# Kernel tuning notes

Measured on AMD Instinct MI355X. Metric: run time of the kernel, lower is better.

The kernel has to match this reference:

```python
import jax, jax.numpy as jnp
import numpy as np

B, T, D = 1, 2048, 2560
H, KV, HD = 8, 4, 256
G = H // KV
S = 8192          # max_seq_len / cache length
PREV = 4096       # tokens already in cache before this chunk
SCALE = 256.0 ** -0.5   # query_pre_attn_scalar ** -0.5
EPS = 1e-6
ROPE_BASE = 10000.0


def _rmsnorm(x, scale):
    xf = x.astype(jnp.float32)
    var = jnp.mean(xf * xf, axis=-1, keepdims=True)
    return xf * jax.lax.rsqrt(var + EPS) * (1.0 + scale)


def _rope(x, cos, sin):
    # x: (b, h, t, hd); cos/sin: (t, hd)
    h = x.shape[-1] // 2
    x1, x2 = x[..., :h], x[..., h:]
    rot = jnp.concatenate([-x2, x1], axis=-1)
    return x * cos[None, None] + rot * sin[None, None]


def setup_inputs() -> dict:
    key = jax.random.key(0)
    ks = jax.random.split(key, 9)
    x = jax.random.normal(ks[0], (B, T, D), jnp.float32)
    Wq = jax.random.normal(ks[1], (H * HD, D), jnp.float32) * 0.02
    Wk = jax.random.normal(ks[2], (KV * HD, D), jnp.float32) * 0.02
    Wv = jax.random.normal(ks[3], (KV * HD, D), jnp.float32) * 0.02
    Wo = jax.random.normal(ks[4], (D, H * HD), jnp.float32) * 0.02
    q_scale = jnp.zeros((HD,), jnp.float32)
    k_scale = jnp.zeros((HD,), jnp.float32)
    k_cache = jax.random.normal(ks[5], (B, S, KV, HD), jnp.float32) * 0.02
    v_cache = jax.random.normal(ks[6], (B, S, KV, HD), jnp.float32) * 0.02
    pos = jnp.arange(PREV, PREV + T, dtype=jnp.int32)
    inv_freq = 1.0 / (ROPE_BASE ** (jnp.arange(0, HD, 2, dtype=jnp.float32) / HD))
    ang = pos.astype(jnp.float32)[:, None] * inv_freq[None, :]   # (T, HD//2)
    cos = jnp.concatenate([jnp.cos(ang), jnp.cos(ang)], axis=-1)  # (T, HD)
    sin = jnp.concatenate([jnp.sin(ang), jnp.sin(ang)], axis=-1)
    # causal mask over the full cache: True = masked out
    mask = jnp.arange(S, dtype=jnp.int32)[None, :] > pos[:, None]  # (T, S) bool
    return dict(x=x, Wq=Wq, Wk=Wk, Wv=Wv, Wo=Wo, q_scale=q_scale,
                k_scale=k_scale, k_cache=k_cache, v_cache=v_cache,
                cos=cos, sin=sin, input_positions=pos, mask=mask)


def reference(x, Wq, Wk, Wv, Wo, q_scale, k_scale, k_cache, v_cache,
              cos, sin, input_positions, mask):
    b, t, _ = x.shape
    q = (x @ Wq.T).reshape(b, t, H, HD).transpose(0, 2, 1, 3)   # (b,H,t,hd)
    k = (x @ Wk.T).reshape(b, t, KV, HD).transpose(0, 2, 1, 3)  # (b,KV,t,hd)
    v = (x @ Wv.T).reshape(b, t, KV, HD).transpose(0, 2, 1, 3)
    q = _rmsnorm(q, q_scale)
    k = _rmsnorm(k, k_scale)
    q = _rope(q, cos, sin)
    k = _rope(k, cos, sin)
    # scatter new K/V into cache at input_positions
    kc = k_cache.at[:, input_positions].set(k.transpose(0, 2, 1, 3))  # (b,S,KV,hd)
    vc = v_cache.at[:, input_positions].set(v.transpose(0, 2, 1, 3))
    # GQA attention without materializing repeated K/V: group heads by KV group
    qg = (q * SCALE).reshape(b, KV, G, t, HD)
    scores = jnp.einsum('bgntd,bsgd->bgnts', qg, kc)  # (b,KV,G,t,S)
    scores = jnp.where(mask, -jnp.inf, scores)        # broadcast (t,S)
    weights = jax.nn.softmax(scores, axis=-1)
    ctx = jnp.einsum('bgnts,bsgd->bgntd', weights, vc)  # (b,KV,G,t,hd)
    ctx = ctx.reshape(b, H, t, HD).transpose(0, 2, 1, 3).reshape(b, t, H * HD)
    return ctx @ Wo.T
```

## Files before the change

### kernel.cpp

```cpp
#include <hip/hip_runtime.h>
#include <hip/hip_bf16.h>

#define T_ 2048
#define D_ 2560
#define H_ 8
#define KV_ 4
#define HD_ 256
#define S_ 8192
#define PREV_ 4096
#define SEFF_ 6144
#define NT_ 192
#define NS_ 2
#define TPS_ 96
#define CHT_ 8
#define SCALE_ 0.0625f
#define LOG2E_ 1.44269504088896f

typedef __attribute__((ext_vector_type(8))) short short8;
typedef __attribute__((ext_vector_type(4))) float floatx4;

__device__ inline short8 ld8(const __hip_bfloat16* p) { return *(const short8*)p; }
__device__ inline short8 ld8(const float* p) {
    float4 a = *(const float4*)p;
    float4 b = *(const float4*)(p + 4);
    union { short8 s; __hip_bfloat16 h[8]; } u;
    u.h[0] = __hip_bfloat16(a.x); u.h[1] = __hip_bfloat16(a.y);
    u.h[2] = __hip_bfloat16(a.z); u.h[3] = __hip_bfloat16(a.w);
    u.h[4] = __hip_bfloat16(b.x); u.h[5] = __hip_bfloat16(b.y);
    u.h[6] = __hip_bfloat16(b.z); u.h[7] = __hip_bfloat16(b.w);
    return u.s;
}

__device__ inline short bfbits(float x) {
    __hip_bfloat16 h(x);
    short s;
    __builtin_memcpy(&s, &h, 2);
    return s;
}

__device__ inline float b2f(short u) {
    unsigned int x = ((unsigned int)(unsigned short)u) << 16;
    float f; __builtin_memcpy(&f, &x, 4); return f;
}

__device__ __forceinline__ void gld_lds(const short* g, short* l) {
    __builtin_amdgcn_global_load_lds(
        (const __attribute__((address_space(1))) unsigned int*)(const void*)g,
        (__attribute__((address_space(3))) unsigned int*)(void*)l,
        16, 0, 0);
}

__device__ __forceinline__ int kslot(int row, int c) {
    int kk = c >> 2, qd = c & 3, hf = row >> 4, lrr = row & 15;
    return (kk * 2 + hf) * 64 + ((qd * 16 + lrr) ^ kk);
}
__device__ __forceinline__ int vslot(int d, int c) {
    int ni = d >> 4, lrr = d & 15;
    return ni * 64 + ((c * 16 + lrr) ^ (ni & 7));
}

__global__ __launch_bounds__(256) void gemm_qkv(const float* __restrict__ A,
                                                const float* __restrict__ Wq,
                                                const float* __restrict__ Wk,
                                                const float* __restrict__ Wv,
                                                float* __restrict__ qo,
                                                float* __restrict__ ko,
                                                float* __restrict__ vo) {
    __shared__ __align__(16) __hip_bfloat16 As[128 * 40];
    __shared__ __align__(16) __hip_bfloat16 Bs[128 * 40];
    const int K = D_;
    const int tid = threadIdx.x;
    const int bm = (int)blockIdx.y * 128, bn = (int)blockIdx.x * 128;
    const int w = tid >> 6, lane = tid & 63, quad = lane >> 4, lr = lane & 15;
    const int wm = (w >> 1) * 64, wn = (w & 1) * 64;
    floatx4 acc[4][4] = {};
    const int row = tid >> 2;
    const int col = (tid & 3) * 8;

    const float* Bp; float* Co; int nb, ldo;
    if (bn < 2048)      { Bp = Wq + (size_t)bn * K;          Co = qo; nb = bn;        ldo = 2048; }
    else if (bn < 3072) { Bp = Wk + (size_t)(bn - 2048) * K; Co = ko; nb = bn - 2048; ldo = 1024; }
    else                { Bp = Wv + (size_t)(bn - 3072) * K; Co = vo; nb = bn - 3072; ldo = 1024; }

    for (int k0 = 0; k0 < K; k0 += 32) {
        __syncthreads();
        for (int p = 0; p < 2; ++p) {
            int r = row + p * 64;
            *(short8*)(&As[r * 40 + col]) = ld8(&A[(size_t)(bm + r) * K + k0 + col]);
            *(short8*)(&Bs[r * 40 + col]) = ld8(&Bp[(size_t)r * K + k0 + col]);
        }
        __syncthreads();
        short8 a[4], b[4];
        for (int mi = 0; mi < 4; ++mi)
            a[mi] = *(const short8*)(&As[(wm + mi * 16 + lr) * 40 + quad * 8]);
        for (int ni = 0; ni < 4; ++ni)
            b[ni] = *(const short8*)(&Bs[(wn + ni * 16 + lr) * 40 + quad * 8]);
        for (int mi = 0; mi < 4; ++mi)
            for (int ni = 0; ni < 4; ++ni)
                acc[mi][ni] = __builtin_amdgcn_mfma_f32_16x16x32_bf16(a[mi], b[ni], acc[mi][ni], 0, 0, 0);
    }
    for (int mi = 0; mi < 4; ++mi)
        for (int ni = 0; ni < 4; ++ni)
            for (int r = 0; r < 4; ++r) {
                int m = bm + wm + mi * 16 + quad * 4 + r;
                int n = nb + wn + ni * 16 + lr;
                Co[(size_t)m * ldo + n] = acc[mi][ni][r];
            }
}

__global__ __launch_bounds__(256) void gemm_wo(const __hip_bfloat16* __restrict__ A,
                                               const float* __restrict__ Bm,
                                               float* __restrict__ C) {
    __shared__ __align__(16) __hip_bfloat16 As[64 * 40];
    __shared__ __align__(16) __hip_bfloat16 Bs[128 * 40];
    const int K = 2048, N = D_;
    const int tid = threadIdx.x;
    const int bm = (int)blockIdx.y * 64, bn = (int)blockIdx.x * 128;
    const int w = tid >> 6, lane = tid & 63, quad = lane >> 4, lr = lane & 15;
    const int wn = w * 32;
    floatx4 acc[4][2] = {};
    const int row = tid >> 2;
    const int col = (tid & 3) * 8;

    for (int k0 = 0; k0 < K; k0 += 32) {
        __syncthreads();
        *(short8*)(&As[row * 40 + col]) = ld8(&A[(size_t)(bm + row) * K + k0 + col]);
        for (int p = 0; p < 2; ++p) {
            int r = row + p * 64;
            *(short8*)(&Bs[r * 40 + col]) = ld8(&Bm[(size_t)(bn + r) * K + k0 + col]);
        }
        __syncthreads();
        short8 a[4], b[2];
        for (int mi = 0; mi < 4; ++mi)
            a[mi] = *(const short8*)(&As[(mi * 16 + lr) * 40 + quad * 8]);
        for (int ni = 0; ni < 2; ++ni)
            b[ni] = *(const short8*)(&Bs[(wn + ni * 16 + lr) * 40 + quad * 8]);
        for (int mi = 0; mi < 4; ++mi)
            for (int ni = 0; ni < 2; ++ni)
                acc[mi][ni] = __builtin_amdgcn_mfma_f32_16x16x32_bf16(a[mi], b[ni], acc[mi][ni], 0, 0, 0);
    }
    for (int mi = 0; mi < 4; ++mi)
        for (int ni = 0; ni < 2; ++ni)
            for (int r = 0; r < 4; ++r) {
                int m = bm + mi * 16 + quad * 4 + r;
                int n = bn + wn + ni * 16 + lr;
                C[(size_t)m * N + n] = acc[mi][ni][r];
            }
}

__global__ __launch_bounds__(256) void norm_rope_q(const float* __restrict__ src,
                                                   const float* __restrict__ scale,
                                                   const float* __restrict__ cosd,
                                                   const float* __restrict__ sind,
                                                   __hip_bfloat16* __restrict__ dst) {
    const int rowid = blockIdx.x;
    const int t = rowid / H_, hh = rowid % H_;
    const int d = threadIdx.x;
    __shared__ float ybuf[256];
    __shared__ float wsum[4];
    float x = src[(size_t)t * (H_ * 256) + hh * 256 + d];
    float ss = x * x;
    for (int m = 1; m < 64; m <<= 1) ss += __shfl_xor(ss, m);
    if ((d & 63) == 0) wsum[d >> 6] = ss;
    __syncthreads();
    float tot = wsum[0] + wsum[1] + wsum[2] + wsum[3];
    float inv = rsqrtf(tot * (1.0f / 256.0f) + 1e-6f);
    float y = x * inv * (1.0f + scale[d]);
    ybuf[d] = y;
    __syncthreads();
    float rot = (d < 128) ? -ybuf[d + 128] : ybuf[d - 128];
    float cv = cosd[(size_t)t * 256 + d];
    float sv = sind[(size_t)t * 256 + d];
    float out = y * cv + rot * sv;
    dst[((size_t)hh * T_ + t) * 256 + d] = __hip_bfloat16(out);
}

__global__ __launch_bounds__(256) void norm_rope_k(const float* __restrict__ src,
                                                   const float* __restrict__ scale,
                                                   const float* __restrict__ cosd,
                                                   const float* __restrict__ sind,
                                                   short* __restrict__ Kp) {
    const int rowid = blockIdx.x;
    const int t = rowid / KV_, g = rowid % KV_;
    const int d = threadIdx.x;
    __shared__ float ybuf[256];
    __shared__ float wsum[4];
    float x = src[(size_t)t * (KV_ * 256) + g * 256 + d];
    float ss = x * x;
    for (int m = 1; m < 64; m <<= 1) ss += __shfl_xor(ss, m);
    if ((d & 63) == 0) wsum[d >> 6] = ss;
    __syncthreads();
    float tot = wsum[0] + wsum[1] + wsum[2] + wsum[3];
    float inv = rsqrtf(tot * (1.0f / 256.0f) + 1e-6f);
    float y = x * inv * (1.0f + scale[d]);
    ybuf[d] = y;
    __syncthreads();
    float rot = (d < 128) ? -ybuf[d + 128] : ybuf[d - 128];
    float cv = cosd[(size_t)t * 256 + d];
    float sv = sind[(size_t)t * 256 + d];
    float out = y * cv + rot * sv;
    const int s = t + PREV_;
    const int tile = s >> 5, row = s & 31;
    Kp[((size_t)(g * NT_ + tile) * 1024 + kslot(row, d >> 3)) * 8 + (d & 7)] = bfbits(out);
}

__global__ __launch_bounds__(256) void merge_k(const float* __restrict__ kin,
                                               short* __restrict__ Kp) {
    const int tile = blockIdx.x;
    const int g = blockIdx.y;
    const int s0 = tile * 32;
    const int tid = threadIdx.x;
    short* dst = Kp + (size_t)(g * NT_ + tile) * 1024 * 8;
    for (int p = 0; p < 4; ++p) {
        int cid = p * 256 + tid;
        int row = cid >> 5, c = cid & 31;
        short8 v = ld8(&kin[((size_t)(s0 + row) * KV_ + g) * 256 + c * 8]);
        *(short8*)&dst[(size_t)kslot(row, c) * 8] = v;
    }
}

__global__ __launch_bounds__(256) void transpose_v(const float* __restrict__ vin,
                                                   const float* __restrict__ vnew,
                                                   short* __restrict__ Vp) {
    __shared__ short tile[64][65];
    const int g = blockIdx.z;
    const int d0 = blockIdx.y * 64;
    const int s0 = blockIdx.x * 64;
    const int tid = threadIdx.x;
    for (int p = 0; p < 16; ++p) {
        int idx = p * 256 + tid;
        int r = idx >> 6, cc = idx & 63;
        int s = s0 + r, d = d0 + cc;
        float v;
        if (s < PREV_) v = vin[((size_t)s * KV_ + g) * 256 + d];
        else           v = vnew[(size_t)(s - PREV_) * 1024 + g * 256 + d];
        tile[r][cc] = bfbits(v);
    }
    __syncthreads();
    for (int p = 0; p < 16; ++p) {
        int idx = p * 256 + tid;
        int r = idx >> 6, cc = idx & 63;
        int s = s0 + cc, d = d0 + r;
        int tl = s >> 5, jj = s & 31;
        Vp[((size_t)(g * NT_ + tl) * 1024 + vslot(d, jj >> 3)) * 8 + (jj & 7)] = tile[cc][r];
    }
}

__global__ void init_bar(unsigned* bar) {
    if (threadIdx.x < 8 * 32) bar[threadIdx.x] = 0u;
}

__device__ __forceinline__ void gbar(unsigned* bar, int myq, unsigned target) {
    __syncthreads();
    if (threadIdx.x == 0) {
        __threadfence();
        atomicAdd(&bar[myq * 32], 1u);
        unsigned sum = 0;
        for (int i = 0; i < 8; ++i)
            sum += __hip_atomic_load(&bar[i * 32], __ATOMIC_RELAXED, __HIP_MEMORY_SCOPE_AGENT);
        while (sum < target) {
            __builtin_amdgcn_s_sleep(8);
            sum = 0;
            for (int i = 0; i < 8; ++i)
                sum += __hip_atomic_load(&bar[i * 32], __ATOMIC_RELAXED, __HIP_MEMORY_SCOPE_AGENT);
        }
    }
    __syncthreads();
}

__global__ __launch_bounds__(256, 2) void attn(const __hip_bfloat16* __restrict__ Qr,
                                               const short* __restrict__ Kp,
                                               const short* __restrict__ Vp,
                                               short* __restrict__ Po,
                                               float* __restrict__ Pm,
                                               float* __restrict__ Pl,
                                               unsigned* __restrict__ bar) {
    __shared__ __align__(16) short Ks[2][8192];
    __shared__ __align__(16) short Vs[2][8192];
    __shared__ __align__(16) short Pls[4][512];
    const int b = (int)blockIdx.x;
    const int h = b >> 6;
    const int jq = (b >> 1) & 31;
    const int ns = b & 1;
    const int g = h >> 1;
    const int qbase = jq * 64;
    const int tid = threadIdx.x;
    const int w = tid >> 6, lane = tid & 63, quad = lane >> 4, lr = lane & 15;
    const int t0 = qbase + w * 16;
    const int myq = b & 7;
    const int rot = b & (CHT_ - 1);

    const short* Qb = (const short*)Qr + ((size_t)h * T_ + t0) * 256;
    const short* Kg = Kp + (size_t)g * NT_ * 8192;
    const short* Vg = Vp + (size_t)g * NT_ * 8192;

    short8 aq[8];
    for (int kk = 0; kk < 8; ++kk)
        aq[kk] = *(const short8*)(&Qb[(size_t)lr * 256 + kk * 32 + quad * 8]);

    floatx4 o[16] = {};
    floatx4 lacc = {0.f, 0.f, 0.f, 0.f};
    float mrow[4] = {-3e38f, -3e38f, -3e38f, -3e38f};
    const float c = SCALE_ * LOG2E_;
    short* pw = &Pls[w][0];
    const short oneb = (short)0x3F80;
    const short8 ones8 = {oneb, oneb, oneb, oneb, oneb, oneb, oneb, oneb};

    const int nf_w = (PREV_ + t0) >> 5;
    const int nf_b = (PREV_ + qbase + 48) >> 5;
    const int cbeg = (ns * TPS_) / CHT_;
    const int cend = cbeg + TPS_ / CHT_;

#define STAGE_TILE(buf, tileidx) do {                                          \
        const short* Kt_ = Kg + (size_t)(tileidx) * 8192;                      \
        const short* Vt_ = Vg + (size_t)(tileidx) * 8192;                      \
        for (int p_ = 0; p_ < 4; ++p_) {                                       \
            gld_lds(Kt_ + (p_ * 256 + w * 64 + lane) * 8,                      \
                    &Ks[buf][(p_ * 256 + w * 64) * 8]);                        \
            gld_lds(Vt_ + (p_ * 256 + w * 64 + lane) * 8,                      \
                    &Vs[buf][(p_ * 256 + w * 64) * 8]);                        \
        }                                                                      \
    } while (0)

    {
        const int tf = cbeg * CHT_ + rot;
        if (tf <= nf_b) STAGE_TILE(0, tf);
    }
    int cur = 0;
    unsigned nbar = 0;
    for (int ci = cbeg; ci < cend; ++ci) {
        for (int i = 0; i < CHT_; ++i) {
            const int tile = ci * CHT_ + ((i + rot) & (CHT_ - 1));
            if (i == 0 && ci > cbeg) { ++nbar; gbar(bar, myq, 512u * nbar); }
            else __syncthreads();
            {
                int ni_ = i + 1, nc_ = ci;
                if (ni_ == CHT_) { ni_ = 0; ++nc_; }
                if (nc_ < cend) {
                    const int nt_ = nc_ * CHT_ + ((ni_ + rot) & (CHT_ - 1));
                    if (nt_ <= nf_b) STAGE_TILE(cur ^ 1, nt_);
                }
            }

            if (tile <= nf_w) {
                const int s0 = tile * 32;
                const bool masked = (tile == nf_w);
                const short* Kb = &Ks[cur][0];
                const short* Vb = &Vs[cur][0];

                floatx4 sc[2];
                __builtin_amdgcn_s_setprio(1);
                for (int half = 0; half < 2; ++half) {
                    floatx4 accs = {0.f, 0.f, 0.f, 0.f};
                    for (int kk = 0; kk < 8; ++kk) {
                        short8 bk = *(const short8*)&Kb[((kk * 2 + half) * 64 + ((quad * 16 + lr) ^ kk)) * 8];
                        accs = __builtin_amdgcn_mfma_f32_16x16x32_bf16(aq[kk], bk, accs, 0, 0, 0);
                    }
                    sc[half] = accs;
                }
                __builtin_amdgcn_s_setprio(0);
                float mnew[4];
                for (int r = 0; r < 4; ++r) {
                    float v0 = sc[0][r] * c, v1 = sc[1][r] * c;
                    if (masked) {
                        int limit = PREV_ + t0 + quad * 4 + r;
                        if (s0 + lr > limit)       v0 = -3e38f;
                        if (s0 + 16 + lr > limit)  v1 = -3e38f;
                    }
                    sc[0][r] = v0; sc[1][r] = v1;
                    float mx = fmaxf(v0, v1);
                    mx = fmaxf(mx, __shfl_xor(mx, 1));
                    mx = fmaxf(mx, __shfl_xor(mx, 2));
                    mx = fmaxf(mx, __shfl_xor(mx, 4));
                    mx = fmaxf(mx, __shfl_xor(mx, 8));
                    mnew[r] = fmaxf(mrow[r], mx);
                }
                float alpha[4];
                for (int r = 0; r < 4; ++r) { alpha[r] = exp2f(mrow[r] - mnew[r]); mrow[r] = mnew[r]; }
                for (int r = 0; r < 4; ++r) {
                    sc[0][r] = exp2f(sc[0][r] - mnew[r]);
                    sc[1][r] = exp2f(sc[1][r] - mnew[r]);
                }
                bool need = (alpha[0] < 1.f) | (alpha[1] < 1.f) | (alpha[2] < 1.f) | (alpha[3] < 1.f);
                if (__any(need)) {
                    for (int ni = 0; ni < 16; ++ni)
                        for (int r = 0; r < 4; ++r) o[ni][r] *= alpha[r];
                    for (int r = 0; r < 4; ++r) lacc[r] *= alpha[r];
                }
                for (int half = 0; half < 2; ++half)
                    for (int r = 0; r < 4; ++r) {
                        int koff2 = half * 16 + lr;
                        pw[((koff2 >> 3) * 16 + quad * 4 + r) * 8 + (koff2 & 7)] = bfbits(sc[half][r]);
                    }
                __asm__ volatile("s_waitcnt lgkmcnt(0)" ::: "memory");
                short8 ap = *(const short8*)&pw[(quad * 16 + lr) * 8];
                __builtin_amdgcn_s_setprio(1);
                lacc = __builtin_amdgcn_mfma_f32_16x16x32_bf16(ap, ones8, lacc, 0, 0, 0);
                for (int ni = 0; ni < 16; ++ni) {
                    short8 bv = *(const short8*)&Vb[(ni * 64 + ((quad * 16 + lr) ^ (ni & 7))) * 8];
                    o[ni] = __builtin_amdgcn_mfma_f32_16x16x32_bf16(ap, bv, o[ni], 0, 0, 0);
                }
                __builtin_amdgcn_s_setprio(0);
            }
            cur ^= 1;
        }
    }
#undef STAGE_TILE

    const int tq = jq * 4 + w;
    const size_t pb16 = (((size_t)h * 128 + tq) * NS_ + ns) * 16;
    const size_t pb = pb16 * 256;
    for (int ni = 0; ni < 16; ++ni) {
        union { unsigned long long u; short s4[4]; } pk;
        for (int r = 0; r < 4; ++r) pk.s4[r] = bfbits(o[ni][r]);
        *(unsigned long long*)&Po[pb + (size_t)ni * 256 + lane * 4] = pk.u;
    }
    if (lr == 0)
        for (int r = 0; r < 4; ++r) {
            Pm[pb16 + quad * 4 + r] = mrow[r];
            Pl[pb16 + quad * 4 + r] = lacc[r];
        }
}

__global__ __launch_bounds__(256) void attn_combine(const short* __restrict__ Po,
                                                    const float* __restrict__ Pm,
                                                    const float* __restrict__ Pl,
                                                    __hip_bfloat16* __restrict__ ctx) {
    const int h = blockIdx.x;
    const int tt = blockIdx.y;
    const int tid = threadIdx.x;
    __shared__ float wgt[NS_][16];
    const size_t b = ((size_t)h * 128 + tt) * NS_;
    if (tid < 16) {
        const int row = tid;
        float m[NS_], l[NS_];
        float M = -3e38f;
        for (int ns = 0; ns < NS_; ++ns) {
            m[ns] = Pm[(b + ns) * 16 + row];
            l[ns] = Pl[(b + ns) * 16 + row];
            M = fmaxf(M, m[ns]);
        }
        float denom = 0.f, wv[NS_];
        for (int ns = 0; ns < NS_; ++ns) {
            wv[ns] = exp2f(m[ns] - M);
            denom += wv[ns] * l[ns];
        }
        float rd = 1.f / denom;
        for (int ns = 0; ns < NS_; ++ns) wgt[ns][row] = wv[ns] * rd;
    }
    __syncthreads();
    const int d = tid;
    const int ni = d >> 4, dl = d & 15;
    for (int row = 0; row < 16; ++row) {
        float acc = 0.f;
        const size_t ib = (size_t)ni * 256 + ((row >> 2) * 16 + dl) * 4 + (row & 3);
        for (int ns = 0; ns < NS_; ++ns)
            acc += wgt[ns][row] * b2f(Po[(b + ns) * 4096 + ib]);
        int t = tt * 16 + row;
        ctx[(size_t)t * (H_ * 256) + h * 256 + d] = __hip_bfloat16(acc);
    }
}

extern "C" void kernel_launch(void* const* d_in, const int* in_sizes, int n_in,
                              void* d_out, int out_size, void* d_ws, size_t ws_size,
                              hipStream_t stream) {
    const float* x       = (const float*)d_in[0];
    const float* Wq      = (const float*)d_in[1];
    const float* Wk      = (const float*)d_in[2];
    const float* Wv      = (const float*)d_in[3];
    const float* Wo      = (const float*)d_in[4];
    const float* q_scale = (const float*)d_in[5];
    const float* k_scale = (const float*)d_in[6];
    const float* k_cache = (const float*)d_in[7];
    const float* v_cache = (const float*)d_in[8];
    const float* cosd    = (const float*)d_in[9];
    const float* sind    = (const float*)d_in[10];
    float* out = (float*)d_out;

    char* p = (char*)d_ws;
    float* q_f32 = (float*)p;            p += (size_t)T_ * 2048 * 4;
    float* k_f32 = (float*)p;            p += (size_t)T_ * 1024 * 4;
    float* v_f32 = (float*)p;            p += (size_t)T_ * 1024 * 4;
    __hip_bfloat16* Qr = (__hip_bfloat16*)p;  p += (size_t)H_ * T_ * 256 * 2;
    short* Kp = (short*)p;               p += (size_t)KV_ * NT_ * 1024 * 8 * 2;
    short* Vp = (short*)p;               p += (size_t)KV_ * NT_ * 1024 * 8 * 2;
    __hip_bfloat16* ctx = (__hip_bfloat16*)p; p += (size_t)T_ * 2048 * 2;
    float* Pm = (float*)p;               p += (size_t)H_ * 128 * NS_ * 16 * 4;
    float* Pl = (float*)p;               p += (size_t)H_ * 128 * NS_ * 16 * 4;
    unsigned* bar = (unsigned*)p;        p += 8 * 32 * sizeof(unsigned);
    short* Po = (short*)d_ws;

    gemm_qkv<<<dim3(32, 16), 256, 0, stream>>>(x, Wq, Wk, Wv, q_f32, k_f32, v_f32);

    norm_rope_q<<<T_ * H_, 256, 0, stream>>>(q_f32, q_scale, cosd, sind, Qr);
    norm_rope_k<<<T_ * KV_, 256, 0, stream>>>(k_f32, k_scale, cosd, sind, Kp);

    merge_k<<<dim3(PREV_ / 32, KV_), 256, 0, stream>>>(k_cache, Kp);
    transpose_v<<<dim3(SEFF_ / 64, HD_ / 64, KV_), 256, 0, stream>>>(v_cache, v_f32, Vp);

    init_bar<<<1, 256, 0, stream>>>(bar);
    attn<<<dim3(512), 256, 0, stream>>>(Qr, Kp, Vp, Po, Pm, Pl, bar);
    attn_combine<<<dim3(H_, 128), 256, 0, stream>>>(Po, Pm, Pl, ctx);

    gemm_wo<<<dim3(20, 32), 256, 0, stream>>>(ctx, Wo, out);
}
```

Baseline: 801.4 us.

## Double attention block size and process two KV tiles per iteration

The attention kernel now runs 256 blocks of 512 threads, each covering 128 query rows instead of 64. Each loop step stages and consumes two 32-key tiles at once, interleaved so the two splits take alternating tile pairs. The old rotated chunk order is gone, and the global barrier now fires every four steps with a lower target and a shorter sleep. The aim is to double the reuse of each staged K/V tile across more warps and halve per-tile sync and softmax overhead. The cost is more LDS and registers per block and possible causal imbalance between blocks.

```diff
diff --git a/kernel.cpp b/kernel.cpp
--- a/kernel.cpp
+++ b/kernel.cpp
@@ -11,8 +11,7 @@
 #define SEFF_ 6144
 #define NT_ 192
 #define NS_ 2
-#define TPS_ 96
-#define CHT_ 8
+#define NJ_ 48
 #define SCALE_ 0.0625f
 #define LOG2E_ 1.44269504088896f
 
@@ -259,7 +258,7 @@
         for (int i = 0; i < 8; ++i)
             sum += __hip_atomic_load(&bar[i * 32], __ATOMIC_RELAXED, __HIP_MEMORY_SCOPE_AGENT);
         while (sum < target) {
-            __builtin_amdgcn_s_sleep(8);
+            __builtin_amdgcn_s_sleep(4);
             sum = 0;
             for (int i = 0; i < 8; ++i)
                 sum += __hip_atomic_load(&bar[i * 32], __ATOMIC_RELAXED, __HIP_MEMORY_SCOPE_AGENT);
@@ -268,33 +267,33 @@
     __syncthreads();
 }
 
-__global__ __launch_bounds__(256, 2) void attn(const __hip_bfloat16* __restrict__ Qr,
+__global__ __launch_bounds__(512, 2) void attn(const __hip_bfloat16* __restrict__ Qr,
                                                const short* __restrict__ Kp,
                                                const short* __restrict__ Vp,
                                                short* __restrict__ Po,
                                                float* __restrict__ Pm,
                                                float* __restrict__ Pl,
                                                unsigned* __restrict__ bar) {
-    __shared__ __align__(16) short Ks[2][8192];
-    __shared__ __align__(16) short Vs[2][8192];
-    __shared__ __align__(16) short Pls[4][512];
+    __shared__ __align__(16) short Ks[2][2][8192];
+    __shared__ __align__(16) short Vs[2][2][8192];
+    __shared__ __align__(16) short Pls[8][1024];
     const int b = (int)blockIdx.x;
-    const int h = b >> 6;
-    const int jq = (b >> 1) & 31;
+    const int h = b >> 5;
+    const int jq = (b >> 1) & 15;
     const int ns = b & 1;
     const int g = h >> 1;
-    const int qbase = jq * 64;
+    const int qbase = jq * 128;
     const int tid = threadIdx.x;
     const int w = tid >> 6, lane = tid & 63, quad = lane >> 4, lr = lane & 15;
     const int t0 = qbase + w * 16;
     const int myq = b & 7;
-    const int rot = b & (CHT_ - 1);
 
     const short* Qb = (const short*)Qr + ((size_t)h * T_ + t0) * 256;
     const short* Kg = Kp + (size_t)g * NT_ * 8192;
     const short* Vg = Vp + (size_t)g * NT_ * 8192;
 
     short8 aq[8];
+#pragma unroll
     for (int kk = 0; kk < 8; ++kk)
         aq[kk] = *(const short8*)(&Qb[(size_t)lr * 256 + kk * 32 + quad * 8]);
 
@@ -307,115 +306,132 @@
     const short8 ones8 = {oneb, oneb, oneb, oneb, oneb, oneb, oneb, oneb};
 
     const int nf_w = (PREV_ + t0) >> 5;
-    const int nf_b = (PREV_ + qbase + 48) >> 5;
-    const int cbeg = (ns * TPS_) / CHT_;
-    const int cend = cbeg + TPS_ / CHT_;
-
-#define STAGE_TILE(buf, tileidx) do {                                          \
-        const short* Kt_ = Kg + (size_t)(tileidx) * 8192;                      \
-        const short* Vt_ = Vg + (size_t)(tileidx) * 8192;                      \
+    const int nf_b = (PREV_ + qbase + 127) >> 5;
+
+#define STAGE_PAIR(buf, ta_) do {                                              \
         for (int p_ = 0; p_ < 4; ++p_) {                                       \
-            gld_lds(Kt_ + (p_ * 256 + w * 64 + lane) * 8,                      \
-                    &Ks[buf][(p_ * 256 + w * 64) * 8]);                        \
-            gld_lds(Vt_ + (p_ * 256 + w * 64 + lane) * 8,                      \
-                    &Vs[buf][(p_ * 256 + w * 64) * 8]);                        \
+            int q_ = w * 4 + p_, tt_ = q_ >> 4, cc_ = q_ & 15;                 \
+            gld_lds(Kg + (size_t)((ta_) + tt_) * 8192 + (cc_ * 64 + lane) * 8, \
+                    &Ks[buf][tt_][cc_ * 512]);                                 \
+            gld_lds(Vg + (size_t)((ta_) + tt_) * 8192 + (cc_ * 64 + lane) * 8, \
+                    &Vs[buf][tt_][cc_ * 512]);                                 \
         }                                                                      \
     } while (0)
 
-    {
-        const int tf = cbeg * CHT_ + rot;
-        if (tf <= nf_b) STAGE_TILE(0, tf);
-    }
+    STAGE_PAIR(0, 2 * ns);
     int cur = 0;
     unsigned nbar = 0;
-    for (int ci = cbeg; ci < cend; ++ci) {
-        for (int i = 0; i < CHT_; ++i) {
-            const int tile = ci * CHT_ + ((i + rot) & (CHT_ - 1));
-            if (i == 0 && ci > cbeg) { ++nbar; gbar(bar, myq, 512u * nbar); }
-            else __syncthreads();
-            {
-                int ni_ = i + 1, nc_ = ci;
-                if (ni_ == CHT_) { ni_ = 0; ++nc_; }
-                if (nc_ < cend) {
-                    const int nt_ = nc_ * CHT_ + ((ni_ + rot) & (CHT_ - 1));
-                    if (nt_ <= nf_b) STAGE_TILE(cur ^ 1, nt_);
-                }
-            }
-
-            if (tile <= nf_w) {
-                const int s0 = tile * 32;
-                const bool masked = (tile == nf_w);
-                const short* Kb = &Ks[cur][0];
-                const short* Vb = &Vs[cur][0];
-
-                floatx4 sc[2];
-                __builtin_amdgcn_s_setprio(1);
+    for (int j = 0; j < NJ_; ++j) {
+        if (j > 0 && (j & 3) == 0) { ++nbar; gbar(bar, myq, 256u * nbar); }
+        else __syncthreads();
+        {
+            const int nta = 4 * (j + 1) + 2 * ns;
+            if (j + 1 < NJ_ && nta <= nf_b) STAGE_PAIR(cur ^ 1, nta);
+        }
+        const int ta = 4 * j + 2 * ns, tb = ta + 1;
+
+        if (ta <= nf_w) {
+            const int s0a = ta * 32, s0b = tb * 32;
+            floatx4 sc[2][2];
+            __builtin_amdgcn_s_setprio(1);
+#pragma unroll
+            for (int st = 0; st < 2; ++st) {
+                const short* Kb = &Ks[cur][st][0];
+#pragma unroll
                 for (int half = 0; half < 2; ++half) {
                     floatx4 accs = {0.f, 0.f, 0.f, 0.f};
+#pragma unroll
                     for (int kk = 0; kk < 8; ++kk) {
                         short8 bk = *(const short8*)&Kb[((kk * 2 + half) * 64 + ((quad * 16 + lr) ^ kk)) * 8];
                         accs = __builtin_amdgcn_mfma_f32_16x16x32_bf16(aq[kk], bk, accs, 0, 0, 0);
                     }
-                    sc[half] = accs;
+                    sc[st][half] = accs;
                 }
-                __builtin_amdgcn_s_setprio(0);
-                float mnew[4];
-                for (int r = 0; r < 4; ++r) {
-                    float v0 = sc[0][r] * c, v1 = sc[1][r] * c;
-                    if (masked) {
-                        int limit = PREV_ + t0 + quad * 4 + r;
-                        if (s0 + lr > limit)       v0 = -3e38f;
-                        if (s0 + 16 + lr > limit)  v1 = -3e38f;
-                    }
-                    sc[0][r] = v0; sc[1][r] = v1;
-                    float mx = fmaxf(v0, v1);
-                    mx = fmaxf(mx, __shfl_xor(mx, 1));
-                    mx = fmaxf(mx, __shfl_xor(mx, 2));
-                    mx = fmaxf(mx, __shfl_xor(mx, 4));
-                    mx = fmaxf(mx, __shfl_xor(mx, 8));
-                    mnew[r] = fmaxf(mrow[r], mx);
+            }
+            __builtin_amdgcn_s_setprio(0);
+            float mnew[4];
+#pragma unroll
+            for (int r = 0; r < 4; ++r) {
+                float v00 = sc[0][0][r] * c, v01 = sc[0][1][r] * c;
+                float v10 = sc[1][0][r] * c, v11 = sc[1][1][r] * c;
+                const int limit = PREV_ + t0 + quad * 4 + r;
+                if (ta >= nf_w) {
+                    if (s0a + lr > limit)       v00 = -3e38f;
+                    if (s0a + 16 + lr > limit)  v01 = -3e38f;
                 }
-                float alpha[4];
-                for (int r = 0; r < 4; ++r) { alpha[r] = exp2f(mrow[r] - mnew[r]); mrow[r] = mnew[r]; }
-                for (int r = 0; r < 4; ++r) {
-                    sc[0][r] = exp2f(sc[0][r] - mnew[r]);
-                    sc[1][r] = exp2f(sc[1][r] - mnew[r]);
+                if (tb >= nf_w) {
+                    if (s0b + lr > limit)       v10 = -3e38f;
+                    if (s0b + 16 + lr > limit)  v11 = -3e38f;
                 }
-                bool need = (alpha[0] < 1.f) | (alpha[1] < 1.f) | (alpha[2] < 1.f) | (alpha[3] < 1.f);
-                if (__any(need)) {
-                    for (int ni = 0; ni < 16; ++ni)
-                        for (int r = 0; r < 4; ++r) o[ni][r] *= alpha[r];
-                    for (int r = 0; r < 4; ++r) lacc[r] *= alpha[r];
-                }
+                sc[0][0][r] = v00; sc[0][1][r] = v01;
+                sc[1][0][r] = v10; sc[1][1][r] = v11;
+                float mx = fmaxf(fmaxf(v00, v01), fmaxf(v10, v11));
+                mx = fmaxf(mx, __shfl_xor(mx, 1));
+                mx = fmaxf(mx, __shfl_xor(mx, 2));
+                mx = fmaxf(mx, __shfl_xor(mx, 4));
+                mx = fmaxf(mx, __shfl_xor(mx, 8));
+                mnew[r] = fmaxf(mrow[r], mx);
+            }
+            float alpha[4];
+#pragma unroll
+            for (int r = 0; r < 4; ++r) { alpha[r] = exp2f(mrow[r] - mnew[r]); mrow[r] = mnew[r]; }
+#pragma unroll
+            for (int r = 0; r < 4; ++r) {
+                sc[0][0][r] = exp2f(sc[0][0][r] - mnew[r]);
+                sc[0][1][r] = exp2f(sc[0][1][r] - mnew[r]);
+                sc[1][0][r] = exp2f(sc[1][0][r] - mnew[r]);
+                sc[1][1][r] = exp2f(sc[1][1][r] - mnew[r]);
+            }
+            bool need = (alpha[0] < 1.f) | (alpha[1] < 1.f) | (alpha[2] < 1.f) | (alpha[3] < 1.f);
+            if (__any(need)) {
+#pragma unroll
+                for (int ni = 0; ni < 16; ++ni)
+#pragma unroll
+                    for (int r = 0; r < 4; ++r) o[ni][r] *= alpha[r];
+#pragma unroll
+                for (int r = 0; r < 4; ++r) lacc[r] *= alpha[r];
+            }
+#pragma unroll
+            for (int st = 0; st < 2; ++st)
+#pragma unroll
                 for (int half = 0; half < 2; ++half)
+#pragma unroll
                     for (int r = 0; r < 4; ++r) {
                         int koff2 = half * 16 + lr;
-                        pw[((koff2 >> 3) * 16 + quad * 4 + r) * 8 + (koff2 & 7)] = bfbits(sc[half][r]);
+                        pw[st * 512 + ((koff2 >> 3) * 16 + quad * 4 + r) * 8 + (koff2 & 7)] = bfbits(sc[st][half][r]);
                     }
-                __asm__ volatile("s_waitcnt lgkmcnt(0)" ::: "memory");
-                short8 ap = *(const short8*)&pw[(quad * 16 + lr) * 8];
-                __builtin_amdgcn_s_setprio(1);
-                lacc = __builtin_amdgcn_mfma_f32_16x16x32_bf16(ap, ones8, lacc, 0, 0, 0);
-                for (int ni = 0; ni < 16; ++ni) {
-                    short8 bv = *(const short8*)&Vb[(ni * 64 + ((quad * 16 + lr) ^ (ni & 7))) * 8];
-                    o[ni] = __builtin_amdgcn_mfma_f32_16x16x32_bf16(ap, bv, o[ni], 0, 0, 0);
-                }
-                __builtin_amdgcn_s_setprio(0);
-            }
-            cur ^= 1;
-        }
-    }
-#undef STAGE_TILE
-
-    const int tq = jq * 4 + w;
+            __asm__ volatile("s_waitcnt lgkmcnt(0)" ::: "memory");
+            short8 ap0 = *(const short8*)&pw[(quad * 16 + lr) * 8];
+            short8 ap1 = *(const short8*)&pw[512 + (quad * 16 + lr) * 8];
+            __builtin_amdgcn_s_setprio(1);
+            lacc = __builtin_amdgcn_mfma_f32_16x16x32_bf16(ap0, ones8, lacc, 0, 0, 0);
+            lacc = __builtin_amdgcn_mfma_f32_16x16x32_bf16(ap1, ones8, lacc, 0, 0, 0);
+#pragma unroll
+            for (int ni = 0; ni < 16; ++ni) {
+                const int vs = (ni * 64 + ((quad * 16 + lr) ^ (ni & 7))) * 8;
+                short8 bv0 = *(const short8*)&Vs[cur][0][vs];
+                o[ni] = __builtin_amdgcn_mfma_f32_16x16x32_bf16(ap0, bv0, o[ni], 0, 0, 0);
+                short8 bv1 = *(const short8*)&Vs[cur][1][vs];
+                o[ni] = __builtin_amdgcn_mfma_f32_16x16x32_bf16(ap1, bv1, o[ni], 0, 0, 0);
+            }
+            __builtin_amdgcn_s_setprio(0);
+        }
+        cur ^= 1;
+    }
+#undef STAGE_PAIR
+
+    const int tq = jq * 8 + w;
     const size_t pb16 = (((size_t)h * 128 + tq) * NS_ + ns) * 16;
     const size_t pb = pb16 * 256;
+#pragma unroll
     for (int ni = 0; ni < 16; ++ni) {
         union { unsigned long long u; short s4[4]; } pk;
+#pragma unroll
         for (int r = 0; r < 4; ++r) pk.s4[r] = bfbits(o[ni][r]);
         *(unsigned long long*)&Po[pb + (size_t)ni * 256 + lane * 4] = pk.u;
     }
     if (lr == 0)
+#pragma unroll
         for (int r = 0; r < 4; ++r) {
             Pm[pb16 + quad * 4 + r] = mrow[r];
             Pl[pb16 + quad * 4 + r] = lacc[r];
@@ -499,7 +515,7 @@
     transpose_v<<<dim3(SEFF_ / 64, HD_ / 64, KV_), 256, 0, stream>>>(v_cache, v_f32, Vp);
 
     init_bar<<<1, 256, 0, stream>>>(bar);
-    attn<<<dim3(512), 256, 0, stream>>>(Qr, Kp, Vp, Po, Pm, Pl, bar);
+    attn<<<dim3(256), 512, 0, stream>>>(Qr, Kp, Vp, Po, Pm, Pl, bar);
     attn_combine<<<dim3(H_, 128), 256, 0, stream>>>(Po, Pm, Pl, ctx);
 
     gemm_wo<<<dim3(20, 32), 256, 0, stream>>>(ctx, Wo, out);
```

New measurement: 649.8 us. 1.23x faster.
